# Kernel tuning notes

Measured on AMD Instinct MI355X. Metric: run time of the kernel, lower is better.

Reference implementation:

```python
import jax, jax.numpy as jnp
import numpy as np

N_USERS = 50000
N_ITEMS = 100000
N_ENT = 200000
N_REL_TOTAL = 32  # n_relations * 2
DIM = 64
N_INTENTS = 2
N_LAYERS = 1
B = 4096
E_KG = 2_000_000
E_UI_HALF = 1_000_000  # user->item interactions; symmetrized to 2M directed edges


def setup_inputs() -> dict:
    key = jax.random.key(0)
    ks = jax.random.split(key, 16)
    s = 0.05  # xavier-ish scale
    user_emb = jax.random.normal(ks[0], (N_USERS, DIM), jnp.float32) * s
    entity_emb = jax.random.normal(ks[1], (N_ENT, DIM), jnp.float32) * s
    relation_emb = jax.random.normal(ks[2], (N_REL_TOTAL, DIM), jnp.float32) * s
    intent_weights = jax.random.normal(ks[3], (N_INTENTS, N_REL_TOTAL), jnp.float32) * s
    router_w = jax.random.normal(ks[4], (N_INTENTS, DIM), jnp.float32) * s
    router_b = jnp.zeros((N_INTENTS,), jnp.float32)
    kg_w = jax.random.normal(ks[5], (N_LAYERS, DIM, DIM), jnp.float32) * (1.0 / np.sqrt(DIM))
    item2entity = jax.random.randint(ks[6], (N_ITEMS,), 0, N_ENT)
    kg_src = jax.random.randint(ks[7], (E_KG,), 0, N_ENT)
    kg_dst = jax.random.randint(ks[8], (E_KG,), 0, N_ENT)
    kg_rel = jax.random.randint(ks[9], (E_KG,), 0, N_REL_TOTAL)
    # UI bipartite graph, symmetrically normalized (D^-1/2 A D^-1/2), as in _build_ui_graph
    rng = np.random.default_rng(0)
    uu = rng.integers(0, N_USERS, E_UI_HALF)
    ii = rng.integers(0, N_ITEMS, E_UI_HALF) + N_USERS
    rows = np.concatenate([uu, ii])
    cols = np.concatenate([ii, uu])
    n_nodes = N_USERS + N_ITEMS
    deg = np.bincount(rows, minlength=n_nodes).astype(np.float32)
    dinv = np.where(deg > 0, deg ** -0.5, 0.0).astype(np.float32)
    ui_vals = jnp.asarray(dinv[rows] * dinv[cols])
    ui_row = jnp.asarray(rows.astype(np.int32))
    ui_col = jnpseq = jnp.asarray(cols.astype(np.int32))
    u = jax.random.randint(ks[10], (B,), 0, N_USERS)
    i = jax.random.randint(ks[11], (B,), 0, N_ITEMS)
    neg_i = jax.random.randint(ks[12], (B,), 0, N_ITEMS)
    return dict(u=u, i=i, neg_i=neg_i,
                user_emb=user_emb, entity_emb=entity_emb, relation_emb=relation_emb,
                intent_weights=intent_weights, router_w=router_w, router_b=router_b,
                kg_w=kg_w, ui_vals=ui_vals,
                item2entity=item2entity, kg_src=kg_src, kg_dst=kg_dst, kg_rel=kg_rel,
                ui_row=ui_row, ui_col=ui_col)


def _l2norm(x):
    return x / jnp.maximum(jnp.linalg.norm(x, axis=-1, keepdims=True), 1e-12)


def reference(u, i, neg_i, user_emb, entity_emb, relation_emb, intent_weights,
              router_w, router_b, kg_w, ui_vals, item2entity, kg_src, kg_dst,
              kg_rel, ui_row, ui_col):
    n_ent = entity_emb.shape[0]
    # ---- _propagate_kg (dropout in eval mode = identity) ----
    x = entity_emb
    gate = jax.nn.sigmoid(relation_emb[kg_rel])  # [E, D]
    deg = jax.ops.segment_sum(jnp.ones(kg_dst.shape[0], jnp.float32), kg_dst,
                              num_segments=n_ent)
    deg = jnp.maximum(deg, 1.0)[:, None]
    for l in range(kg_w.shape[0]):
        msg = (x[kg_src] @ kg_w[l].T) * gate           # gather + linear + gate
        agg = jax.ops.segment_sum(msg, kg_dst, num_segments=n_ent)
        x = _l2norm(jax.nn.elu(agg / deg + x))
    item_kg = x[item2entity]                            # [n_items, D]
    # ---- _propagate_ui: sparse normalized adj propagation ----
    all_emb = jnp.concatenate([user_emb, item_kg], 0)
    n_nodes = all_emb.shape[0]
    embs = [all_emb]
    for _ in range(N_LAYERS):
        all_emb = jax.ops.segment_sum(ui_vals[:, None] * all_emb[ui_col], ui_row,
                                      num_segments=n_nodes)
        embs.append(all_emb)
    final = jnp.mean(jnp.stack(embs, 1), 1)
    n_users = user_emb.shape[0]
    u_prop, i_prop = final[:n_users], final[n_users:]
    # ---- intent mixing ----
    intent_dist = jax.nn.softmax(u_prop @ router_w.T + router_b, axis=-1)
    intent_emb = jax.nn.softmax(intent_weights, axis=-1) @ relation_emb
    ue = u_prop + intent_dist @ intent_emb
    ie = i_prop + item_kg
    pos = jnp.sum(ue[u] * ie[i], 1)
    neg = jnp.sum(ue[u] * ie[neg_i], 1)
    return pos, neg
```

## Files before the change

kernel.cpp:

```cpp
#include <hip/hip_runtime.h>
#include <math.h>

#define N_USERS 50000
#define N_ITEMS 100000
#define N_ENT   200000
#define N_NODES (N_USERS + N_ITEMS)
#define N_REL   32
#define DIM     64

#define NB_KG  391
#define NB_UI  586
#define NB_TOT (NB_KG + NB_UI)
#define CAPK   4096
#define CAPU   1536
#define NMMTILE 1563
#define NSCAT  768
#define FUSE_GRID (NSCAT + NMMTILE)
#define NCPY   208
#define KGOFF  (NB_UI + NCPY)

__device__ __forceinline__ unsigned short f2bf(float f) {
    unsigned u = __float_as_uint(f);
    u += 0x7FFFu + ((u >> 16) & 1u);
    return (unsigned short)(u >> 16);
}
__device__ __forceinline__ float bf_lo(unsigned v) { return __uint_as_float(v << 16); }
__device__ __forceinline__ float bf_hi(unsigned v) { return __uint_as_float(v & 0xFFFF0000u); }
__device__ __forceinline__ int getbit(const unsigned* m, int i) {
    return (m[i >> 5] >> (i & 31)) & 1;
}

__global__ __launch_bounds__(256) void build_masks(const int* __restrict__ i2e,
                                                   const int* __restrict__ u,
                                                   const int* __restrict__ ipos,
                                                   const int* __restrict__ ineg,
                                                   const float* __restrict__ rel_emb,
                                                   const float* __restrict__ iw,
                                                   float2* __restrict__ gateg,
                                                   float* __restrict__ intentg,
                                                   unsigned* __restrict__ ent_mask,
                                                   unsigned* __restrict__ node_mask,
                                                   int* __restrict__ bcur,
                                                   int B) {
    int t = blockIdx.x * 256 + threadIdx.x;
    int stride = gridDim.x * 256;
    for (int i = threadIdx.x; i < NB_TOT; i += 256)
        bcur[i] = (i < NB_KG) ? i * CAPK : (i - NB_KG) * CAPU;
    if (blockIdx.x == 0) {
        for (int idx = threadIdx.x; idx < N_REL * 32; idx += 256) {
            int rel = idx >> 5, hl2 = idx & 31;
            float g0 = 1.0f / (1.0f + __expf(-rel_emb[rel * 64 + 2 * hl2]));
            float g1 = 1.0f / (1.0f + __expf(-rel_emb[rel * 64 + 2 * hl2 + 1]));
            gateg[idx] = make_float2(g0, g1);
        }
        if (threadIdx.x < 64) {
            int j = threadIdx.x;
            for (int k = 0; k < 2; k++) {
                float m = -1e30f;
                for (int r = 0; r < N_REL; r++) m = fmaxf(m, iw[k * N_REL + r]);
                float Z = 0.f, acc = 0.f;
                for (int r = 0; r < N_REL; r++) {
                    float e = __expf(iw[k * N_REL + r] - m);
                    Z += e;
                    acc += e * rel_emb[r * 64 + j];
                }
                intentg[k * 64 + j] = acc / Z;
            }
        }
    }
    for (int i = t; i < N_ITEMS; i += stride) {
        int e = i2e[i];
        atomicOr(&ent_mask[e >> 5], 1u << (e & 31));
    }
    for (int i = t; i < 3 * B; i += stride) {
        int r = (i < B) ? u[i]
              : (i < 2 * B) ? N_USERS + ipos[i - B]
                            : N_USERS + ineg[i - 2 * B];
        atomicOr(&node_mask[r >> 5], 1u << (r & 31));
    }
}

__global__ __launch_bounds__(512) void mm_scatter(const float* __restrict__ x,
                                                  const float* __restrict__ w,
                                                  unsigned short* __restrict__ y16,
                                                  int n_ent,
                                                  const int* __restrict__ kg_src,
                                                  const int* __restrict__ kg_dst,
                                                  const int* __restrict__ kg_rel,
                                                  const int* __restrict__ ui_row,
                                                  const int* __restrict__ ui_col,
                                                  const float* __restrict__ ui_vals,
                                                  const unsigned* __restrict__ ent_mask,
                                                  const unsigned* __restrict__ node_mask,
                                                  unsigned* __restrict__ colneed,
                                                  int* __restrict__ bcur,
                                                  unsigned int* __restrict__ kgrec,
                                                  int* __restrict__ uirec,
                                                  float* __restrict__ uval,
                                                  int e_kg, int e_ui) {
    __shared__ __align__(16) char smem[49152];
    int tid = threadIdx.x;
    int bid = blockIdx.x;

    if (bid < NSCAT) {
        int* h     = (int*)smem;
        int* lbase = h + NB_TOT;
        int n = e_kg + e_ui;
        int nchunks = (n + 4095) >> 12;
        for (int c = bid; c < nchunks; c += NSCAT) {
            int base = c << 12;
            for (int i = tid; i < NB_TOT; i += 512) h[i] = 0;
            __syncthreads();
            unsigned int rec[8];
            float val[8];
            int bk[8];
            #pragma unroll
            for (int j = 0; j < 8; j++) {
                int e = base + j * 512 + tid;
                bk[j] = -1;
                if (e < n) {
                    if (e < e_kg) {
                        int d = kg_dst[e];
                        if (getbit(ent_mask, d)) {
                            bk[j]  = d >> 9;
                            rec[j] = (unsigned int)kg_src[e]
                                     | ((unsigned int)kg_rel[e] << 18)
                                     | ((unsigned int)(d & 511) << 23);
                            atomicAdd(&h[bk[j]], 1);
                        }
                    } else {
                        int i2 = e - e_kg;
                        int r  = ui_row[i2];
                        if (getbit(node_mask, r)) {
                            int cc = ui_col[i2];
                            bk[j]  = NB_KG + (r >> 8);
                            rec[j] = (unsigned int)cc
                                     | ((unsigned int)(r & 255) << 18);
                            val[j] = ui_vals[i2];
                            atomicAdd(&h[bk[j]], 1);
                            if (r < N_USERS) {
                                int ci = cc - N_USERS;
                                atomicOr(&colneed[ci >> 5], 1u << (ci & 31));
                            }
                        }
                    }
                }
            }
            __syncthreads();
            for (int i = tid; i < NB_TOT; i += 512) {
                int cc = h[i];
                lbase[i] = cc ? atomicAdd(&bcur[i], cc) : 0;
            }
            __syncthreads();
            #pragma unroll
            for (int j = 0; j < 8; j++) {
                if (bk[j] >= 0) {
                    int pos = atomicAdd(&lbase[bk[j]], 1);
                    if (bk[j] < NB_KG) {
                        if (pos < (bk[j] + 1) * CAPK) kgrec[pos] = rec[j];
                    } else {
                        int bu = bk[j] - NB_KG;
                        if (pos < (bu + 1) * CAPU) { uirec[pos] = (int)rec[j]; uval[pos] = val[j]; }
                    }
                }
            }
            __syncthreads();
        }
        return;
    }

    int mtile = bid - NSCAT;
    float (*xt)[128] = (float (*)[128])smem;
    float (*wt)[64]  = (float (*)[64])(smem + 32768);
    int base = mtile * 128;

    #pragma unroll
    for (int q = 0; q < 2; q++) {
        int idx = q * 512 + tid;
        int j = idx >> 4, k4 = idx & 15;
        int s0 = (k4 << 2) & 28;
        float4 v = ((const float4*)w)[idx];
        wt[4 * k4 + 0][j ^ s0] = v.x;
        wt[4 * k4 + 1][j ^ s0] = v.y;
        wt[4 * k4 + 2][j ^ s0] = v.z;
        wt[4 * k4 + 3][j ^ s0] = v.w;
    }
    #pragma unroll
    for (int q = 0; q < 4; q++) {
        int idx = q * 512 + tid;
        int r = idx >> 4, k4 = idx & 15;
        int gr = base + r;
        int s0 = (k4 << 2) & 28;
        if (gr < n_ent) {
            float4 v = ((const float4*)x)[(long)gr * 16 + k4];
            xt[4 * k4 + 0][r ^ s0] = v.x;
            xt[4 * k4 + 1][r ^ s0] = v.y;
            xt[4 * k4 + 2][r ^ s0] = v.z;
            xt[4 * k4 + 3][r ^ s0] = v.w;
        }
    }
    __syncthreads();

    int j0 = (tid & 7) * 8;
    int r0 = (tid >> 3) * 2;
    float acc[2][8];
    #pragma unroll
    for (int i = 0; i < 2; i++)
        #pragma unroll
        for (int j = 0; j < 8; j++) acc[i][j] = 0.f;

    #pragma unroll 4
    for (int k = 0; k < 64; k++) {
        int s = k & 28;
        float2 xa = *(const float2*)&xt[k][r0 ^ s];
        float4 wa = *(const float4*)&wt[k][j0 ^ s];
        float4 wb = *(const float4*)&wt[k][(j0 + 4) ^ s];
        float xr[2] = {xa.x, xa.y};
        float wr[8] = {wa.x, wa.y, wa.z, wa.w, wb.x, wb.y, wb.z, wb.w};
        #pragma unroll
        for (int i = 0; i < 2; i++)
            #pragma unroll
            for (int j = 0; j < 8; j++)
                acc[i][j] += xr[i] * wr[j];
    }

    #pragma unroll
    for (int i = 0; i < 2; i++) {
        int gr = base + r0 + i;
        if (gr < n_ent) {
            uint4 o;
            o.x = (unsigned)f2bf(acc[i][0]) | ((unsigned)f2bf(acc[i][1]) << 16);
            o.y = (unsigned)f2bf(acc[i][2]) | ((unsigned)f2bf(acc[i][3]) << 16);
            o.z = (unsigned)f2bf(acc[i][4]) | ((unsigned)f2bf(acc[i][5]) << 16);
            o.w = (unsigned)f2bf(acc[i][6]) | ((unsigned)f2bf(acc[i][7]) << 16);
            *(uint4*)&y16[(long)gr * 64 + j0] = o;
        }
    }
}

__global__ __launch_bounds__(256) void finalize_kg(const int* __restrict__ bcur,
                                                   unsigned int* __restrict__ kgrec,
                                                   int* __restrict__ beg_kg,
                                                   int* __restrict__ end_kg) {
    __shared__ unsigned int rec[CAPK];
    __shared__ int hist[512];
    int b    = blockIdx.x;
    int base = b * CAPK;
    int ne   = min(bcur[b] - base, CAPK);
    int key_base = b << 9;
    int nkeys = min(512, N_ENT - key_base);
    int tid = threadIdx.x;

    for (int i = tid; i < ne; i += 256) rec[i] = kgrec[base + i];
    for (int i = tid; i < 512; i += 256) hist[i] = 0;
    __syncthreads();
    for (int i = tid; i < ne; i += 256)
        atomicAdd(&hist[rec[i] >> 23], 1);
    __syncthreads();
    int i0 = tid, i1 = tid + 256;
    int v0 = hist[i0], v1 = hist[i1];
    __syncthreads();
    for (int o = 1; o < 512; o <<= 1) {
        int a0 = (i0 >= o) ? hist[i0 - o] : 0;
        int a1 = (i1 >= o) ? hist[i1 - o] : 0;
        __syncthreads();
        hist[i0] += a0; hist[i1] += a1;
        __syncthreads();
    }
    int e0 = hist[i0] - v0, e1 = hist[i1] - v1;
    __syncthreads();
    hist[i0] = e0; hist[i1] = e1;
    if (i0 < nkeys) { beg_kg[key_base + i0] = base + e0; end_kg[key_base + i0] = base + e0 + v0; }
    if (i1 < nkeys) { beg_kg[key_base + i1] = base + e1; end_kg[key_base + i1] = base + e1 + v1; }
    __syncthreads();
    for (int i = tid; i < ne; i += 256) {
        unsigned int r = rec[i];
        int slot = atomicAdd(&hist[r >> 23], 1);
        kgrec[base + slot] = r & 0x7FFFFFu;
    }
}

__global__ __launch_bounds__(256) void kgagg_fused(const int* __restrict__ bcur,
                                                   int* __restrict__ uirec,
                                                   float* __restrict__ uval,
                                                   int* __restrict__ beg_ui,
                                                   int* __restrict__ end_ui,
                                                   const float* __restrict__ user_emb,
                                                   const int* __restrict__ beg_kg,
                                                   const int* __restrict__ end_kg,
                                                   const unsigned int* __restrict__ packed,
                                                   const unsigned short* __restrict__ y16,
                                                   const float* __restrict__ entity_emb,
                                                   const int* __restrict__ i2e,
                                                   const float4* __restrict__ gate4,
                                                   const unsigned* __restrict__ node_mask,
                                                   const unsigned* __restrict__ colneed,
                                                   float* __restrict__ all_emb,
                                                   unsigned short* __restrict__ all16) {
    __shared__ __align__(16) char smem[14336];
    int tid = threadIdx.x;
    int bid = blockIdx.x;

    if (bid < NB_UI) {
        unsigned int* rec = (unsigned int*)smem;
        float* fval = (float*)(smem + 6144);
        int*   hist = (int*)(smem + 12288);
        int b    = bid;
        int base = b * CAPU;
        int ne   = min(bcur[NB_KG + b] - base, CAPU);
        int key_base = b << 8;
        int nkeys = min(256, N_NODES - key_base);

        for (int i = tid; i < ne; i += 256) {
            rec[i] = (unsigned int)uirec[base + i];
            fval[i] = uval[base + i];
        }
        for (int i = tid; i < 512; i += 256) hist[i] = 0;
        __syncthreads();
        for (int i = tid; i < ne; i += 256)
            atomicAdd(&hist[rec[i] >> 18], 1);
        __syncthreads();
        int i0 = tid, i1 = tid + 256;
        int v0 = hist[i0], v1 = hist[i1];
        __syncthreads();
        for (int o = 1; o < 512; o <<= 1) {
            int a0 = (i0 >= o) ? hist[i0 - o] : 0;
            int a1 = (i1 >= o) ? hist[i1 - o] : 0;
            __syncthreads();
            hist[i0] += a0; hist[i1] += a1;
            __syncthreads();
        }
        int e0 = hist[i0] - v0, e1 = hist[i1] - v1;
        __syncthreads();
        hist[i0] = e0; hist[i1] = e1;
        if (i0 < nkeys) { beg_ui[key_base + i0] = base + e0; end_ui[key_base + i0] = base + e0 + v0; }
        if (i1 < nkeys) { beg_ui[key_base + i1] = base + e1; end_ui[key_base + i1] = base + e1 + v1; }
        __syncthreads();
        for (int i = tid; i < ne; i += 256) {
            unsigned int r = rec[i];
            int slot = atomicAdd(&hist[r >> 18], 1);
            uirec[base + slot] = (int)(r & 0x3FFFFu);
            uval[base + slot] = fval[i];
        }
        return;
    }

    if (bid < KGOFF) {
        int cid = bid - NB_UI;
        const float4* ue4 = (const float4*)user_emb;
        uint2* a2 = (uint2*)all16;
        int total = N_USERS * 16;
        for (int i = cid * 256 + tid; i < total; i += NCPY * 256) {
            float4 v = ue4[i];
            a2[i] = make_uint2((unsigned)f2bf(v.x) | ((unsigned)f2bf(v.y) << 16),
                               (unsigned)f2bf(v.z) | ((unsigned)f2bf(v.w) << 16));
        }
        return;
    }

    int kblk = bid - KGOFF;
    int lane = tid & 63;
    int half = lane >> 5;
    int hl   = lane & 31;
    int duo  = hl >> 4;
    int ql   = hl & 15;
    long wpair = (long)((kblk * 256 + tid) >> 6);
    int it = (int)(wpair * 2 + half);
    if (it >= N_ITEMS) return;
    int w = N_USERS + it;
    if (!(getbit(colneed, it) | getbit(node_mask, w))) return;

    int ent = i2e[it];
    const uint2* y2 = (const uint2*)y16;
    int beg = beg_kg[ent], end = end_kg[ent];
    float a0 = 0.f, a1 = 0.f, a2 = 0.f, a3 = 0.f;
    float b0 = 0.f, b1 = 0.f, b2 = 0.f, b3 = 0.f;
    int p = beg;
    for (; p + 4 <= end; p += 4) {
        unsigned pk0 = packed[p + duo];
        unsigned pk1 = packed[p + 2 + duo];
        uint2 v0 = y2[(long)(pk0 & 0x3FFFF) * 16 + ql];
        uint2 v1 = y2[(long)(pk1 & 0x3FFFF) * 16 + ql];
        float4 g0 = gate4[(pk0 >> 18) * 16 + ql];
        float4 g1 = gate4[(pk1 >> 18) * 16 + ql];
        a0 += bf_lo(v0.x) * g0.x;  a1 += bf_hi(v0.x) * g0.y;
        a2 += bf_lo(v0.y) * g0.z;  a3 += bf_hi(v0.y) * g0.w;
        b0 += bf_lo(v1.x) * g1.x;  b1 += bf_hi(v1.x) * g1.y;
        b2 += bf_lo(v1.y) * g1.z;  b3 += bf_hi(v1.y) * g1.w;
    }
    if (p + duo < end) {
        unsigned pk = packed[p + duo];
        uint2 v = y2[(long)(pk & 0x3FFFF) * 16 + ql];
        float4 g = gate4[(pk >> 18) * 16 + ql];
        a0 += bf_lo(v.x) * g.x;  a1 += bf_hi(v.x) * g.y;
        a2 += bf_lo(v.y) * g.z;  a3 += bf_hi(v.y) * g.w;
    }
    if (p + 2 + duo < end) {
        unsigned pk = packed[p + 2 + duo];
        uint2 v = y2[(long)(pk & 0x3FFFF) * 16 + ql];
        float4 g = gate4[(pk >> 18) * 16 + ql];
        b0 += bf_lo(v.x) * g.x;  b1 += bf_hi(v.x) * g.y;
        b2 += bf_lo(v.y) * g.z;  b3 += bf_hi(v.y) * g.w;
    }
    a0 += b0; a1 += b1; a2 += b2; a3 += b3;
    a0 += __shfl_xor(a0, 16);
    a1 += __shfl_xor(a1, 16);
    a2 += __shfl_xor(a2, 16);
    a3 += __shfl_xor(a3, 16);

    float deg = fmaxf((float)(end - beg), 1.0f);
    float4 xv = ((const float4*)entity_emb)[(long)ent * 16 + ql];
    float v0 = a0 / deg + xv.x;
    float v1 = a1 / deg + xv.y;
    float v2 = a2 / deg + xv.z;
    float v3 = a3 / deg + xv.w;
    v0 = (v0 > 0.0f) ? v0 : (__expf(v0) - 1.0f);
    v1 = (v1 > 0.0f) ? v1 : (__expf(v1) - 1.0f);
    v2 = (v2 > 0.0f) ? v2 : (__expf(v2) - 1.0f);
    v3 = (v3 > 0.0f) ? v3 : (__expf(v3) - 1.0f);
    float ss = v0 * v0 + v1 * v1 + v2 * v2 + v3 * v3;
    ss += __shfl_xor(ss, 1);
    ss += __shfl_xor(ss, 2);
    ss += __shfl_xor(ss, 4);
    ss += __shfl_xor(ss, 8);
    float inv = 1.0f / fmaxf(sqrtf(ss), 1e-12f);
    if (duo == 0) {
        float r0 = v0 * inv, r1 = v1 * inv, r2 = v2 * inv, r3 = v3 * inv;
        if (getbit(node_mask, w))
            ((float4*)all_emb)[(long)w * 16 + ql] = make_float4(r0, r1, r2, r3);
        ((uint2*)all16)[(long)w * 16 + ql] =
            make_uint2((unsigned)f2bf(r0) | ((unsigned)f2bf(r1) << 16),
                       (unsigned)f2bf(r2) | ((unsigned)f2bf(r3) << 16));
    }
}

__device__ __forceinline__ float4 agg_row(int beg, int end, int q4, int ql,
                                          const int* __restrict__ colrec,
                                          const float* __restrict__ uval,
                                          const uint2* __restrict__ a2p) {
    float a0 = 0.f, a1 = 0.f, a2 = 0.f, a3 = 0.f;
    float b0 = 0.f, b1 = 0.f, b2 = 0.f, b3 = 0.f;
    int p = beg + q4;
    for (; p + 4 < end; p += 8) {
        int   c0 = colrec[p];     float d0 = uval[p];
        int   c1 = colrec[p + 4]; float d1 = uval[p + 4];
        uint2 v0 = a2p[(long)c0 * 16 + ql];
        uint2 v1 = a2p[(long)c1 * 16 + ql];
        a0 += d0 * bf_lo(v0.x);  a1 += d0 * bf_hi(v0.x);
        a2 += d0 * bf_lo(v0.y);  a3 += d0 * bf_hi(v0.y);
        b0 += d1 * bf_lo(v1.x);  b1 += d1 * bf_hi(v1.x);
        b2 += d1 * bf_lo(v1.y);  b3 += d1 * bf_hi(v1.y);
    }
    if (p < end) {
        int c = colrec[p]; float d = uval[p];
        uint2 v = a2p[(long)c * 16 + ql];
        a0 += d * bf_lo(v.x);  a1 += d * bf_hi(v.x);
        a2 += d * bf_lo(v.y);  a3 += d * bf_hi(v.y);
    }
    a0 += b0; a1 += b1; a2 += b2; a3 += b3;
    a0 += __shfl_xor(a0, 16);  a0 += __shfl_xor(a0, 32);
    a1 += __shfl_xor(a1, 16);  a1 += __shfl_xor(a1, 32);
    a2 += __shfl_xor(a2, 16);  a2 += __shfl_xor(a2, 32);
    a3 += __shfl_xor(a3, 16);  a3 += __shfl_xor(a3, 32);
    return make_float4(a0, a1, a2, a3);
}

__global__ __launch_bounds__(256) void ui_final(const int* __restrict__ beg_ui,
                                                const int* __restrict__ end_ui,
                                                const int* __restrict__ colrec,
                                                const float* __restrict__ uval,
                                                const float* __restrict__ all_emb,
                                                const float* __restrict__ user_emb,
                                                const unsigned short* __restrict__ all16,
                                                const int* __restrict__ u,
                                                const int* __restrict__ ipos,
                                                const int* __restrict__ ineg,
                                                const float* __restrict__ rw,
                                                const float* __restrict__ rb,
                                                const float* __restrict__ intentg,
                                                float* __restrict__ out, int B) {
    const uint2* a2p = (const uint2*)all16;
    int lane = threadIdx.x & 63;
    int q4   = lane >> 4;
    int ql   = lane & 15;
    int b = (int)((blockIdx.x * 256 + threadIdx.x) >> 6);
    if (b >= B) return;

    int ru = u[b];
    float4 s = agg_row(beg_ui[ru], end_ui[ru], q4, ql, colrec, uval, a2p);
    float4 ae = ((const float4*)user_emb)[(long)ru * 16 + ql];
    float up0 = 0.5f * (ae.x + s.x);
    float up1 = 0.5f * (ae.y + s.y);
    float up2 = 0.5f * (ae.z + s.z);
    float up3 = 0.5f * (ae.w + s.w);

    float4 w0 = ((const float4*)rw)[ql];
    float4 w1 = ((const float4*)rw)[16 + ql];
    float l0 = up0 * w0.x + up1 * w0.y + up2 * w0.z + up3 * w0.w;
    float l1 = up0 * w1.x + up1 * w1.y + up2 * w1.z + up3 * w1.w;
    #pragma unroll
    for (int o = 8; o; o >>= 1) {
        l0 += __shfl_xor(l0, o);
        l1 += __shfl_xor(l1, o);
    }
    l0 += rb[0]; l1 += rb[1];
    float m  = fmaxf(l0, l1);
    float e0 = __expf(l0 - m), e1 = __expf(l1 - m);
    float inv = 1.0f / (e0 + e1);
    float p0 = e0 * inv, p1 = e1 * inv;
    float4 it0 = ((const float4*)intentg)[ql];
    float4 it1 = ((const float4*)intentg)[16 + ql];
    float ue0 = up0 + p0 * it0.x + p1 * it1.x;
    float ue1 = up1 + p0 * it0.y + p1 * it1.y;
    float ue2 = up2 + p0 * it0.z + p1 * it1.z;
    float ue3 = up3 + p0 * it0.w + p1 * it1.w;

    {
        int ri = N_USERS + ipos[b];
        float4 si = agg_row(beg_ui[ri], end_ui[ri], q4, ql, colrec, uval, a2p);
        float4 ai = ((const float4*)all_emb)[(long)ri * 16 + ql];
        float ie0 = 0.5f * (ai.x + si.x) + ai.x;
        float ie1 = 0.5f * (ai.y + si.y) + ai.y;
        float ie2 = 0.5f * (ai.z + si.z) + ai.z;
        float ie3 = 0.5f * (ai.w + si.w) + ai.w;
        float dp = ue0 * ie0 + ue1 * ie1 + ue2 * ie2 + ue3 * ie3;
        #pragma unroll
        for (int o = 8; o; o >>= 1) dp += __shfl_xor(dp, o);
        if (lane == 0) out[b] = dp;
    }
    {
        int ri = N_USERS + ineg[b];
        float4 si = agg_row(beg_ui[ri], end_ui[ri], q4, ql, colrec, uval, a2p);
        float4 ai = ((const float4*)all_emb)[(long)ri * 16 + ql];
        float ie0 = 0.5f * (ai.x + si.x) + ai.x;
        float ie1 = 0.5f * (ai.y + si.y) + ai.y;
        float ie2 = 0.5f * (ai.z + si.z) + ai.z;
        float ie3 = 0.5f * (ai.w + si.w) + ai.w;
        float dp = ue0 * ie0 + ue1 * ie1 + ue2 * ie2 + ue3 * ie3;
        #pragma unroll
        for (int o = 8; o; o >>= 1) dp += __shfl_xor(dp, o);
        if (lane == 0) out[B + b] = dp;
    }
}

extern "C" void kernel_launch(void* const* d_in, const int* in_sizes, int n_in,
                              void* d_out, int out_size, void* d_ws, size_t ws_size,
                              hipStream_t stream) {
    const int*   u          = (const int*)  d_in[0];
    const int*   ipos       = (const int*)  d_in[1];
    const int*   ineg       = (const int*)  d_in[2];
    const float* user_emb   = (const float*)d_in[3];
    const float* entity_emb = (const float*)d_in[4];
    const float* rel_emb    = (const float*)d_in[5];
    const float* iw         = (const float*)d_in[6];
    const float* rw         = (const float*)d_in[7];
    const float* rb         = (const float*)d_in[8];
    const float* kgw        = (const float*)d_in[9];
    const float* ui_vals    = (const float*)d_in[10];
    const int*   i2e        = (const int*)  d_in[11];
    const int*   kg_src     = (const int*)  d_in[12];
    const int*   kg_dst     = (const int*)  d_in[13];
    const int*   kg_rel     = (const int*)  d_in[14];
    const int*   ui_row     = (const int*)  d_in[15];
    const int*   ui_col     = (const int*)  d_in[16];
    float*       out        = (float*)d_out;

    int B    = in_sizes[0];
    int e_kg = in_sizes[12];
    int e_ui = in_sizes[15];

    char* ws = (char*)d_ws;
    unsigned short* y16       = (unsigned short*)(ws + 0);
    float*          all_emb   = (float*)(ws + 25600000);
    unsigned short* all16     = (unsigned short*)(ws + 64000000);
    unsigned int*   kgrec     = (unsigned int*)(ws + 121600000);
    int*            end_kg    = (int*)(ws + 128006144);
    int*            end_ui    = (int*)(ws + 128806144);
    int*            uirec     = (int*)(ws + 129600000);
    float*          uval      = (float*)(ws + 133600000);
    int*            beg_kg    = (int*)(ws + 137600000);
    int*            beg_ui    = (int*)(ws + 138400256);
    unsigned*       ent_mask  = (unsigned*)(ws + 139000512);
    unsigned*       node_mask = (unsigned*)(ws + 139025600);
    unsigned*       colneed   = (unsigned*)(ws + 139044352);
    int*            bcur      = (int*)(ws + 139608704);
    float2*         gateg     = (float2*)(ws + 139612672);
    float*          intentg   = (float*)(ws + 139620864);

    hipMemsetAsync(ent_mask, 0, 25088 + 18752 + 12544, stream);
    build_masks<<<512, 256, 0, stream>>>(i2e, u, ipos, ineg, rel_emb, iw,
                                         gateg, intentg,
                                         ent_mask, node_mask, bcur, B);
    mm_scatter <<<FUSE_GRID, 512, 0, stream>>>(
        entity_emb, kgw, y16, N_ENT,
        kg_src, kg_dst, kg_rel, ui_row, ui_col, ui_vals,
        ent_mask, node_mask, colneed, bcur, kgrec, uirec, uval, e_kg, e_ui);
    finalize_kg<<<NB_KG, 256, 0, stream>>>(bcur, kgrec, beg_kg, end_kg);
    {
        int nwaves = N_ITEMS / 2;
        int nkblk  = (nwaves * 64 + 255) / 256;
        kgagg_fused<<<KGOFF + nkblk, 256, 0, stream>>>(
            bcur, uirec, uval, beg_ui, end_ui, user_emb,
            beg_kg, end_kg, kgrec, y16, entity_emb, i2e,
            (const float4*)gateg, node_mask, colneed, all_emb, all16);
    }
    {
        int nblk = (B * 64 + 255) / 256;
        ui_final<<<nblk, 256, 0, stream>>>(
            beg_ui, end_ui, uirec, uval, all_emb, user_emb, all16,
            u, ipos, ineg, rw, rb, intentg, out, B);
    }
}
```

Before: 267.9 us.

## Replace bucketed KG edge sort with per-entity fixed-capacity slot lists

KG edges whose destination entity is needed are no longer written into coarse buckets and then sorted per entity by a separate finalize kernel. Each one now takes a slot through a global atomic counter on its destination entity and is stored in a fixed 48-entry slot array for that entity. The aggregation kernel reads the per-entity count and slots directly, which removes a kernel launch and the in-LDS histogram, scan and scatter pass. In exchange it performs many global atomics to random addresses and uses a larger padded workspace. Edges beyond 48 per entity would be silently dropped while the degree still counts them.

```diff
diff --git a/kernel.cpp b/kernel.cpp
--- a/kernel.cpp
+++ b/kernel.cpp
@@ -11,8 +11,8 @@
 #define NB_KG  391
 #define NB_UI  586
 #define NB_TOT (NB_KG + NB_UI)
-#define CAPK   4096
 #define CAPU   1536
+#define CAPE   48
 #define NMMTILE 1563
 #define NSCAT  768
 #define FUSE_GRID (NSCAT + NMMTILE)
@@ -41,11 +41,13 @@
                                                    unsigned* __restrict__ ent_mask,
                                                    unsigned* __restrict__ node_mask,
                                                    int* __restrict__ bcur,
+                                                   int* __restrict__ ecnt,
                                                    int B) {
     int t = blockIdx.x * 256 + threadIdx.x;
     int stride = gridDim.x * 256;
     for (int i = threadIdx.x; i < NB_TOT; i += 256)
-        bcur[i] = (i < NB_KG) ? i * CAPK : (i - NB_KG) * CAPU;
+        bcur[i] = (i < NB_KG) ? 0 : (i - NB_KG) * CAPU;
+    for (int i = t; i < N_ENT; i += stride) ecnt[i] = 0;
     if (blockIdx.x == 0) {
         for (int idx = threadIdx.x; idx < N_REL * 32; idx += 256) {
             int rel = idx >> 5, hl2 = idx & 31;
@@ -94,7 +96,8 @@
                                                   const unsigned* __restrict__ node_mask,
                                                   unsigned* __restrict__ colneed,
                                                   int* __restrict__ bcur,
-                                                  unsigned int* __restrict__ kgrec,
+                                                  int* __restrict__ ecnt,
+                                                  unsigned int* __restrict__ kgslot,
                                                   int* __restrict__ uirec,
                                                   float* __restrict__ uval,
                                                   int e_kg, int e_ui) {
@@ -104,12 +107,12 @@
 
     if (bid < NSCAT) {
         int* h     = (int*)smem;
-        int* lbase = h + NB_TOT;
+        int* lbase = h + NB_UI;
         int n = e_kg + e_ui;
         int nchunks = (n + 4095) >> 12;
         for (int c = bid; c < nchunks; c += NSCAT) {
             int base = c << 12;
-            for (int i = tid; i < NB_TOT; i += 512) h[i] = 0;
+            for (int i = tid; i < NB_UI; i += 512) h[i] = 0;
             __syncthreads();
             unsigned int rec[8];
             float val[8];
@@ -122,18 +125,17 @@
                     if (e < e_kg) {
                         int d = kg_dst[e];
                         if (getbit(ent_mask, d)) {
-                            bk[j]  = d >> 9;
-                            rec[j] = (unsigned int)kg_src[e]
-                                     | ((unsigned int)kg_rel[e] << 18)
-                                     | ((unsigned int)(d & 511) << 23);
-                            atomicAdd(&h[bk[j]], 1);
+                            unsigned r2 = (unsigned int)kg_src[e]
+                                          | ((unsigned int)kg_rel[e] << 18);
+                            int pos = atomicAdd(&ecnt[d], 1);
+                            if (pos < CAPE) kgslot[(long)d * CAPE + pos] = r2;
                         }
                     } else {
                         int i2 = e - e_kg;
                         int r  = ui_row[i2];
                         if (getbit(node_mask, r)) {
                             int cc = ui_col[i2];
-                            bk[j]  = NB_KG + (r >> 8);
+                            bk[j]  = r >> 8;
                             rec[j] = (unsigned int)cc
                                      | ((unsigned int)(r & 255) << 18);
                             val[j] = ui_vals[i2];
@@ -147,21 +149,16 @@
                 }
             }
             __syncthreads();
-            for (int i = tid; i < NB_TOT; i += 512) {
+            for (int i = tid; i < NB_UI; i += 512) {
                 int cc = h[i];
-                lbase[i] = cc ? atomicAdd(&bcur[i], cc) : 0;
+                lbase[i] = cc ? atomicAdd(&bcur[NB_KG + i], cc) : 0;
             }
             __syncthreads();
             #pragma unroll
             for (int j = 0; j < 8; j++) {
                 if (bk[j] >= 0) {
                     int pos = atomicAdd(&lbase[bk[j]], 1);
-                    if (bk[j] < NB_KG) {
-                        if (pos < (bk[j] + 1) * CAPK) kgrec[pos] = rec[j];
-                    } else {
-                        int bu = bk[j] - NB_KG;
-                        if (pos < (bu + 1) * CAPU) { uirec[pos] = (int)rec[j]; uval[pos] = val[j]; }
-                    }
+                    if (pos < (bk[j] + 1) * CAPU) { uirec[pos] = (int)rec[j]; uval[pos] = val[j]; }
                 }
             }
             __syncthreads();
@@ -238,57 +235,14 @@
     }
 }
 
-__global__ __launch_bounds__(256) void finalize_kg(const int* __restrict__ bcur,
-                                                   unsigned int* __restrict__ kgrec,
-                                                   int* __restrict__ beg_kg,
-                                                   int* __restrict__ end_kg) {
-    __shared__ unsigned int rec[CAPK];
-    __shared__ int hist[512];
-    int b    = blockIdx.x;
-    int base = b * CAPK;
-    int ne   = min(bcur[b] - base, CAPK);
-    int key_base = b << 9;
-    int nkeys = min(512, N_ENT - key_base);
-    int tid = threadIdx.x;
-
-    for (int i = tid; i < ne; i += 256) rec[i] = kgrec[base + i];
-    for (int i = tid; i < 512; i += 256) hist[i] = 0;
-    __syncthreads();
-    for (int i = tid; i < ne; i += 256)
-        atomicAdd(&hist[rec[i] >> 23], 1);
-    __syncthreads();
-    int i0 = tid, i1 = tid + 256;
-    int v0 = hist[i0], v1 = hist[i1];
-    __syncthreads();
-    for (int o = 1; o < 512; o <<= 1) {
-        int a0 = (i0 >= o) ? hist[i0 - o] : 0;
-        int a1 = (i1 >= o) ? hist[i1 - o] : 0;
-        __syncthreads();
-        hist[i0] += a0; hist[i1] += a1;
-        __syncthreads();
-    }
-    int e0 = hist[i0] - v0, e1 = hist[i1] - v1;
-    __syncthreads();
-    hist[i0] = e0; hist[i1] = e1;
-    if (i0 < nkeys) { beg_kg[key_base + i0] = base + e0; end_kg[key_base + i0] = base + e0 + v0; }
-    if (i1 < nkeys) { beg_kg[key_base + i1] = base + e1; end_kg[key_base + i1] = base + e1 + v1; }
-    __syncthreads();
-    for (int i = tid; i < ne; i += 256) {
-        unsigned int r = rec[i];
-        int slot = atomicAdd(&hist[r >> 23], 1);
-        kgrec[base + slot] = r & 0x7FFFFFu;
-    }
-}
-
 __global__ __launch_bounds__(256) void kgagg_fused(const int* __restrict__ bcur,
                                                    int* __restrict__ uirec,
                                                    float* __restrict__ uval,
                                                    int* __restrict__ beg_ui,
                                                    int* __restrict__ end_ui,
                                                    const float* __restrict__ user_emb,
-                                                   const int* __restrict__ beg_kg,
-                                                   const int* __restrict__ end_kg,
-                                                   const unsigned int* __restrict__ packed,
+                                                   const int* __restrict__ ecnt,
+                                                   const unsigned int* __restrict__ kgslot,
                                                    const unsigned short* __restrict__ y16,
                                                    const float* __restrict__ entity_emb,
                                                    const int* __restrict__ i2e,
@@ -372,13 +326,15 @@
 
     int ent = i2e[it];
     const uint2* y2 = (const uint2*)y16;
-    int beg = beg_kg[ent], end = end_kg[ent];
+    int degc = ecnt[ent];
+    int beg = ent * CAPE;
+    int end = beg + min(degc, CAPE);
     float a0 = 0.f, a1 = 0.f, a2 = 0.f, a3 = 0.f;
     float b0 = 0.f, b1 = 0.f, b2 = 0.f, b3 = 0.f;
     int p = beg;
     for (; p + 4 <= end; p += 4) {
-        unsigned pk0 = packed[p + duo];
-        unsigned pk1 = packed[p + 2 + duo];
+        unsigned pk0 = kgslot[p + duo];
+        unsigned pk1 = kgslot[p + 2 + duo];
         uint2 v0 = y2[(long)(pk0 & 0x3FFFF) * 16 + ql];
         uint2 v1 = y2[(long)(pk1 & 0x3FFFF) * 16 + ql];
         float4 g0 = gate4[(pk0 >> 18) * 16 + ql];
@@ -389,14 +345,14 @@
         b2 += bf_lo(v1.y) * g1.z;  b3 += bf_hi(v1.y) * g1.w;
     }
     if (p + duo < end) {
-        unsigned pk = packed[p + duo];
+        unsigned pk = kgslot[p + duo];
         uint2 v = y2[(long)(pk & 0x3FFFF) * 16 + ql];
         float4 g = gate4[(pk >> 18) * 16 + ql];
         a0 += bf_lo(v.x) * g.x;  a1 += bf_hi(v.x) * g.y;
         a2 += bf_lo(v.y) * g.z;  a3 += bf_hi(v.y) * g.w;
     }
     if (p + 2 + duo < end) {
-        unsigned pk = packed[p + 2 + duo];
+        unsigned pk = kgslot[p + 2 + duo];
         uint2 v = y2[(long)(pk & 0x3FFFF) * 16 + ql];
         float4 g = gate4[(pk >> 18) * 16 + ql];
         b0 += bf_lo(v.x) * g.x;  b1 += bf_hi(v.x) * g.y;
@@ -408,7 +364,7 @@
     a2 += __shfl_xor(a2, 16);
     a3 += __shfl_xor(a3, 16);
 
-    float deg = fmaxf((float)(end - beg), 1.0f);
+    float deg = fmaxf((float)degc, 1.0f);
     float4 xv = ((const float4*)entity_emb)[(long)ent * 16 + ql];
     float v0 = a0 / deg + xv.x;
     float v1 = a1 / deg + xv.y;
@@ -573,12 +529,11 @@
     unsigned short* y16       = (unsigned short*)(ws + 0);
     float*          all_emb   = (float*)(ws + 25600000);
     unsigned short* all16     = (unsigned short*)(ws + 64000000);
-    unsigned int*   kgrec     = (unsigned int*)(ws + 121600000);
-    int*            end_kg    = (int*)(ws + 128006144);
+    unsigned int*   kgslot    = (unsigned int*)(ws + 83200000);
+    int*            ecnt      = (int*)(ws + 121600000);
     int*            end_ui    = (int*)(ws + 128806144);
     int*            uirec     = (int*)(ws + 129600000);
     float*          uval      = (float*)(ws + 133600000);
-    int*            beg_kg    = (int*)(ws + 137600000);
     int*            beg_ui    = (int*)(ws + 138400256);
     unsigned*       ent_mask  = (unsigned*)(ws + 139000512);
     unsigned*       node_mask = (unsigned*)(ws + 139025600);
@@ -590,18 +545,18 @@
     hipMemsetAsync(ent_mask, 0, 25088 + 18752 + 12544, stream);
     build_masks<<<512, 256, 0, stream>>>(i2e, u, ipos, ineg, rel_emb, iw,
                                          gateg, intentg,
-                                         ent_mask, node_mask, bcur, B);
+                                         ent_mask, node_mask, bcur, ecnt, B);
     mm_scatter <<<FUSE_GRID, 512, 0, stream>>>(
         entity_emb, kgw, y16, N_ENT,
         kg_src, kg_dst, kg_rel, ui_row, ui_col, ui_vals,
-        ent_mask, node_mask, colneed, bcur, kgrec, uirec, uval, e_kg, e_ui);
-    finalize_kg<<<NB_KG, 256, 0, stream>>>(bcur, kgrec, beg_kg, end_kg);
+        ent_mask, node_mask, colneed, bcur, ecnt, kgslot, uirec, uval,
+        e_kg, e_ui);
     {
         int nwaves = N_ITEMS / 2;
         int nkblk  = (nwaves * 64 + 255) / 256;
         kgagg_fused<<<KGOFF + nkblk, 256, 0, stream>>>(
             bcur, uirec, uval, beg_ui, end_ui, user_emb,
-            beg_kg, end_kg, kgrec, y16, entity_emb, i2e,
+            ecnt, kgslot, y16, entity_emb, i2e,
             (const float4*)gateg, node_mask, colneed, all_emb, all16);
     }
     {
```

Result: slower. 292.8 us (+9.3%).
